# Kernel optimization log

Measured on AMD Instinct MI355X. Metric: run time of the kernel, lower is better.

Reference implementation:

```python
import jax, jax.numpy as jnp
import numpy as np

B, N, DIM, H, DH = 2, 1024, 2048, 16, 128
MAX_POS = 16
QK_SCALE = 10.0  # qk_norm_scale (replaces dim_head**-0.5 when qk_norm=True)
NEG = -1e30  # large negative mask value (sigmoid -> 0, softmax -> 0)

def rotate_half(x):
    # interleaved pair rotation: '... (d r) -> ... d r', r=2
    shape = x.shape
    xr = x.reshape(shape[:-1] + (shape[-1] // 2, 2))
    x1, x2 = xr[..., 0], xr[..., 1]
    return jnp.stack((-x2, x1), axis=-1).reshape(shape)

def setup_inputs() -> dict:
    key = jax.random.key(0)
    ks = jax.random.split(key, 10)
    # proper rotary frequencies, repeat-interleaved to match rotate_half's pair layout
    half = DH // 2
    inv_freq = 1.0 / (10000.0 ** (np.arange(half, dtype=np.float32) / half))
    freqs = np.repeat(np.outer(np.arange(N, dtype=np.float32), inv_freq), 2, axis=-1)  # [N, DH]
    sd = 0.02
    return {
        'x': jax.random.normal(ks[0], (B, N, DIM), jnp.float32),
        'rotary_freqs': jnp.asarray(freqs),
        'w_q': jax.random.normal(ks[1], (DIM, H * DH), jnp.float32) * sd,
        'w_k': jax.random.normal(ks[2], (DIM, H * DH), jnp.float32) * sd,
        'w_v': jax.random.normal(ks[3], (DIM, H * DH), jnp.float32) * sd,
        'cope_emb': jax.random.normal(ks[4], (MAX_POS, DH), jnp.float32) * sd,  # CoPE pos_emb (nonzero for testing)
        'th_pre': jnp.eye(H, dtype=jnp.float32) + jax.random.normal(ks[5], (H, H), jnp.float32) * sd,
        'th_post': jnp.eye(H, dtype=jnp.float32) + jax.random.normal(ks[6], (H, H), jnp.float32) * sd,
        'w_vgate': jax.random.normal(ks[7], (DIM, H * DH), jnp.float32) * sd,
        'b_vgate': jnp.full((H * DH,), 10.0, jnp.float32),
        'w_hgate': jax.random.normal(ks[8], (DIM, H), jnp.float32) * sd,
        'b_hgate': jnp.full((H,), 10.0, jnp.float32),
        'w_out': jax.random.normal(ks[9], (H * DH, DIM), jnp.float32) * sd,
    }

def reference(x, rotary_freqs, w_q, w_k, w_v, cope_emb, th_pre, th_post, w_vgate, b_vgate, w_hgate, b_hgate, w_out):
    b, n, _ = x.shape
    to_heads = lambda t: t.reshape(b, n, H, DH).transpose(0, 2, 1, 3)  # b h n d
    q = to_heads(x @ w_q)
    k = to_heads(x @ w_k)
    v = to_heads(x @ w_v)
    # qk l2-norm (groups=1), then fixed qk_norm_scale
    q = q / jnp.maximum(jnp.linalg.norm(q, axis=-1, keepdims=True), 1e-12)
    k = k / jnp.maximum(jnp.linalg.norm(k, axis=-1, keepdims=True), 1e-12)
    # rotary embedding (scale=1, rot_dim == dim_head)
    cos, sin = jnp.cos(rotary_freqs), jnp.sin(rotary_freqs)
    q = q * cos + rotate_half(q) * sin
    k = k * cos + rotate_half(k) * sin
    sim = jnp.einsum('bhid,bhjd->bhij', q, k) * QK_SCALE
    sim = jnp.einsum('hg,bgij->bhij', th_pre, sim)  # pre-softmax talking heads (1x1 conv over heads)
    causal = jnp.triu(jnp.ones((n, n), dtype=bool), 1)
    sim = jnp.where(causal, NEG, sim)
    # ---- CoPE (linear interpolation path) ----
    gates = jax.nn.sigmoid(sim)  # masked entries -> 0
    pos = jnp.flip(jnp.cumsum(jnp.flip(gates, -1), axis=-1), -1)  # reverse cumsum over j
    pos = jnp.minimum(pos, MAX_POS - 1.0)
    logits_int = jnp.einsum('bhnd,pd->bhnp', q, cope_emb)
    pos_floor = jnp.floor(pos)
    w_interp = pos - pos_floor
    lc = jnp.take_along_axis(logits_int, jnp.ceil(pos).astype(jnp.int32), axis=-1)
    lf = jnp.take_along_axis(logits_int, pos_floor.astype(jnp.int32), axis=-1)
    sim = sim + lc * w_interp + lf * (1.0 - w_interp)
    # ------------------------------------------
    attn = jax.nn.softmax(sim, axis=-1)
    attn = jnp.einsum('hg,bgij->bhij', th_post, attn)  # post-softmax talking heads
    out = jnp.einsum('bhij,bhjd->bhid', attn, v)
    # per-head value gate
    head_gate = jax.nn.sigmoid(x @ w_hgate + b_hgate)  # b n h
    out = out * head_gate.transpose(0, 2, 1)[..., None]
    out = out.transpose(0, 2, 1, 3).reshape(b, n, H * DH)
    # elementwise value gate (sigmoid, bias init 10)
    out = out * jax.nn.sigmoid(x @ w_vgate + b_vgate)
    return out @ w_out
```

## Files before the change

kernel.cpp:

```cpp
#include <hip/hip_runtime.h>
#include <hip/hip_fp16.h>

typedef unsigned short u16;
typedef __attribute__((ext_vector_type(4))) float f32x4;
typedef __attribute__((ext_vector_type(8))) _Float16 f16x8;
typedef __attribute__((ext_vector_type(4))) _Float16 f16x4;
typedef __attribute__((ext_vector_type(8))) unsigned short u16x8;
typedef __attribute__((ext_vector_type(4))) unsigned short u16x4;

#define DEVI __device__ __forceinline__
#define MASKV (-1000.0f)

DEVI u16 f2h(float f){ __half h = __float2half(f); return __half_as_ushort(h); }
DEVI float h2f(u16 v){ return __half2float(__ushort_as_half(v)); }
DEVI float sigm(float s){ float e = __expf(-fabsf(s)); return (s >= 0.f) ? 1.f/(1.f+e) : e/(1.f+e); }

DEVI void async16(const void* g, void* l){
  __builtin_amdgcn_global_load_lds((__attribute__((address_space(1))) const unsigned int*)g,
                                   (__attribute__((address_space(3))) unsigned int*)l, 16, 0, 0);
}

struct Acc { f32x4 a[4][4]; };
DEVI void acc_zero(Acc& a){
  f32x4 z = {0.f,0.f,0.f,0.f};
  #pragma unroll
  for (int i=0;i<4;i++)
    #pragma unroll
    for (int j=0;j<4;j++) a.a[i][j] = z;
}

DEVI void gemm_core(const u16* __restrict__ A, int lda, const u16* __restrict__ Bt, int ldb,
                    int K, u16* As, u16* Bs, Acc& acc, int tid)
{
  int w = tid >> 6, l = tid & 63;
  int q = l >> 4, m = l & 15;
  int wm = w & 1, wn = w >> 1;
  for (int k0 = 0; k0 < K; k0 += 32){
    __syncthreads();
    #pragma unroll
    for (int p = 0; p < 2; p++){
      int row = w*32 + p*16 + (l>>2);
      async16(A  + (size_t)row*lda + k0 + (l&3)*8, As + (w*32 + p*16)*32);
      async16(Bt + (size_t)row*ldb + k0 + (l&3)*8, Bs + (w*32 + p*16)*32);
    }
    __syncthreads();
    f16x8 af[4], bf[4];
    #pragma unroll
    for (int t = 0; t < 4; t++){
      af[t] = *(const f16x8*)(As + (wm*64 + t*16 + m)*32 + q*8);
      bf[t] = *(const f16x8*)(Bs + (wn*64 + t*16 + m)*32 + q*8);
    }
    #pragma unroll
    for (int i = 0; i < 4; i++)
      #pragma unroll
      for (int j = 0; j < 4; j++)
        acc.a[i][j] = __builtin_amdgcn_mfma_f32_16x16x32_f16(af[i], bf[j], acc.a[i][j], 0, 0, 0);
  }
}

struct PrepArgs {
  const float* src[7];
  u16* dst[7];
  int C[7];
};
__global__ __launch_bounds__(256) void k_prep(PrepArgs p){
  __shared__ u16 t[32][33];
  int z = blockIdx.z;
  if (z == 0){
    int i = ((blockIdx.y*64 + blockIdx.x)*256 + threadIdx.x)*4;
    f32x4 v = *(const f32x4*)(p.src[0] + i);
    u16x4 o;
    #pragma unroll
    for (int z2=0; z2<4; z2++) o[z2] = f2h(v[z2]);
    *(u16x4*)(p.dst[0] + i) = o;
    return;
  }
  const float* src = p.src[z]; u16* dst = p.dst[z];
  int R = 2048, C = p.C[z];
  int c0 = blockIdx.x*32, r0 = blockIdx.y*32;
  if (c0 >= C) return;
  int tx = threadIdx.x & 31, ty = threadIdx.x >> 5;
  #pragma unroll
  for (int i = ty; i < 32; i += 8){
    int r = r0 + i, c = c0 + tx;
    if (r < R && c < C) t[i][tx] = f2h(src[(size_t)r*C + c]);
  }
  __syncthreads();
  #pragma unroll
  for (int i = ty; i < 32; i += 8){
    int rr = c0 + i, cc = r0 + tx;
    if (rr < C && cc < R) dst[(size_t)rr*R + cc] = t[tx][i];
  }
}

__global__ __launch_bounds__(256) void k_transpose_h(const u16* __restrict__ src, u16* __restrict__ dst,
    int R, int C, long sps, long dps){
  __shared__ u16 t[32][33];
  src += (size_t)blockIdx.z * sps; dst += (size_t)blockIdx.z * dps;
  int c0 = blockIdx.x*32, r0 = blockIdx.y*32;
  int tx = threadIdx.x & 31, ty = threadIdx.x >> 5;
  #pragma unroll
  for (int i = ty; i < 32; i += 8){
    int r = r0 + i, c = c0 + tx;
    if (r < R && c < C) t[i][tx] = src[(size_t)r*C + c];
  }
  __syncthreads();
  #pragma unroll
  for (int i = ty; i < 32; i += 8){
    int rr = c0 + i, cc = r0 + tx;
    if (rr < C && cc < R) dst[(size_t)rr*R + cc] = t[tx][i];
  }
}

struct ProjArgs {
  const u16* xh;
  const u16* wT0; const u16* wT1; const u16* wT2; const u16* wT3;
  u16* q; u16* k; u16* v; u16* vg;
  const float* bvg;
};
__global__ __launch_bounds__(256) void k_proj(ProjArgs p){
  __shared__ __align__(16) u16 As[4096];
  __shared__ __align__(16) u16 Bs[4096];
  int z = blockIdx.z;
  const u16* wT = (z==0) ? p.wT0 : (z==1) ? p.wT1 : (z==2) ? p.wT2 : p.wT3;
  int tid = threadIdx.x;
  Acc acc; acc_zero(acc);
  const u16* A  = p.xh + (size_t)blockIdx.x*128*2048;
  const u16* Bt = wT   + (size_t)blockIdx.y*128*2048;
  gemm_core(A, 2048, Bt, 2048, 2048, As, Bs, acc, tid);
  int w = tid>>6, l = tid&63, q4 = l>>4, m = l&15, wm = w&1, wn = w>>1;
  #pragma unroll
  for (int ti=0; ti<4; ti++)
  #pragma unroll
  for (int tj=0; tj<4; tj++)
  #pragma unroll
  for (int r=0; r<4; r++){
    int trow = blockIdx.x*128 + wm*64 + ti*16 + q4*4 + r;
    int col  = blockIdx.y*128 + wn*64 + tj*16 + m;
    float v = acc.a[ti][tj][r];
    if (z == 3){
      float sg = sigm(v + p.bvg[col]);
      p.vg[(size_t)trow*2048 + col] = f2h(sg);
    } else {
      int b = trow >> 10, i = trow & 1023, h = col >> 7, d = col & 127;
      u16* dst = (z==0) ? p.q : (z==1) ? p.k : p.v;
      dst[(((size_t)(b*16 + h))*1024 + i)*128 + d] = f2h(v);
    }
  }
}

__global__ __launch_bounds__(256) void k_hgate(const u16* __restrict__ xh, const u16* __restrict__ whgT,
    const float* __restrict__ bhg, float* __restrict__ hg){
  __shared__ float red[4][256];
  int tid = threadIdx.x, w = tid>>6, l = tid&63, q = l>>4, m = l&15;
  int t0 = blockIdx.x*16;
  f32x4 acc = {0.f,0.f,0.f,0.f};
  const u16* xr = xh   + (size_t)(t0 + m)*2048 + w*512;
  const u16* br = whgT + (size_t)m*2048 + w*512;
  #pragma unroll 4
  for (int k = 0; k < 512; k += 32){
    f16x8 a = *(const f16x8*)(xr + k + q*8);
    f16x8 b = *(const f16x8*)(br + k + q*8);
    acc = __builtin_amdgcn_mfma_f32_16x16x32_f16(a, b, acc, 0, 0, 0);
  }
  #pragma unroll
  for (int r = 0; r < 4; r++) red[w][(q*4+r)*16 + m] = acc[r];
  __syncthreads();
  float v = red[0][tid] + red[1][tid] + red[2][tid] + red[3][tid];
  int tl = tid >> 4, h = tid & 15;
  hg[(size_t)(t0 + tl)*16 + h] = sigm(v + bhg[h]);
}

__global__ __launch_bounds__(256) void k_normrope(u16* __restrict__ qb, u16* __restrict__ kb,
    const float* __restrict__ freqs, const float* __restrict__ cope, float* __restrict__ L){
  __shared__ float ce[2048];
  int tid = threadIdx.x;
  for (int i2 = tid; i2 < 2048; i2 += 256) ce[i2] = cope[i2];
  __syncthreads();
  int w = tid >> 6, l = tid & 63;
  int r = blockIdx.x*4 + w;
  int isq = (r < 32768) ? 1 : 0;
  int rr = isq ? r : r - 32768;
  int i = rr & 1023;
  u16* base = (isq ? qb : kb) + (size_t)rr*128;
  float v0 = h2f(base[2*l]), v1 = h2f(base[2*l+1]);
  float ss = v0*v0 + v1*v1;
  #pragma unroll
  for (int off = 1; off < 64; off <<= 1) ss += __shfl_xor(ss, off);
  float rn = 1.f / fmaxf(sqrtf(ss), 1e-12f);
  v0 *= rn; v1 *= rn;
  float f = freqs[i*128 + 2*l];
  float sn, cs; sincosf(f, &sn, &cs);
  float o0 = v0*cs - v1*sn, o1 = v1*cs + v0*sn;
  base[2*l] = f2h(o0); base[2*l+1] = f2h(o1);
  if (isq){
    #pragma unroll
    for (int p = 0; p < 16; p++){
      float part = o0*ce[p*128 + 2*l] + o1*ce[p*128 + 2*l + 1];
      #pragma unroll
      for (int off = 1; off < 64; off <<= 1) part += __shfl_xor(part, off);
      if (l == p) L[(size_t)rr*16 + p] = part;
    }
  }
}

__global__ __launch_bounds__(256) void k_qk(const u16* __restrict__ qb, const u16* __restrict__ kb,
    u16* __restrict__ S){
  __shared__ __align__(16) u16 As[4096];
  __shared__ __align__(16) u16 Bs[4096];
  int tile = blockIdx.x, bh = blockIdx.y;
  int it = 0;
  #pragma unroll
  for (int t2 = 1; t2 < 8; t2++) if (tile >= (t2*(t2+1))/2) it = t2;
  int jt = tile - (it*(it+1))/2;
  const u16* A  = qb + (size_t)bh*131072 + (size_t)it*16384;
  const u16* Bt = kb + (size_t)bh*131072 + (size_t)jt*16384;
  Acc acc; acc_zero(acc);
  gemm_core(A, 128, Bt, 128, 128, As, Bs, acc, threadIdx.x);
  int tid = threadIdx.x, w = tid>>6, l = tid&63, q = l>>4, m = l&15, wm = w&1, wn = w>>1;
  u16* dst = S + ((size_t)bh*36 + tile)*16384;
  #pragma unroll
  for (int ti=0; ti<4; ti++)
  #pragma unroll
  for (int tj=0; tj<4; tj++)
  #pragma unroll
  for (int r=0; r<4; r++){
    int iloc = wm*64 + ti*16 + q*4 + r;
    int jloc = wn*64 + tj*16 + m;
    float v = acc.a[ti][tj][r] * 10.f;
    if (jt*128 + jloc > it*128 + iloc) v = MASKV;
    dst[(size_t)iloc*128 + jloc] = f2h(v);
  }
}

struct CopeArgs { const u16* S; const float* L; const float* thpre; u16* Sout; float* ml; };
__global__ __launch_bounds__(1024) void k_cope(CopeArgs pa){
  __shared__ u16 raw[16*276];
  __shared__ float thsh[256];
  __shared__ float Lsh[1024];
  int b = blockIdx.y;
  int i0 = (int)(gridDim.x - 1 - blockIdx.x) * 4;
  int tid = threadIdx.x, w = tid>>6, l = tid&63;
  int h = w;
  if (tid < 256) thsh[tid] = pa.thpre[tid];
  Lsh[tid] = pa.L[ ((size_t)((b*16 + (tid>>6))*1024) + i0 + ((tid>>4)&3))*16 + (tid&15) ];
  __syncthreads();
  float th_r[16];
  #pragma unroll
  for (int g = 0; g < 16; g++) th_r[g] = thsh[h*16 + g];
  int ii = l >> 4, j0 = (l & 15)*4;
  int i = i0 + ii, it1 = i >> 7, iloc = i & 127;
  const float* Lrow = Lsh + h*64 + ii*16;
  float carry = 0.f, mrun = -1e30f, lrun = 0.f;
  int tmax = (i0 + 3) >> 6;
  for (int t = tmax; t >= 0; t--){
    int jt1 = (t*64) >> 7, jo = (t*64) & 127;
    __syncthreads();
    {
      int e = tid*4;
      int g = e >> 8, r = e & 255;
      int si = r >> 6, j = r & 63;
      int irow = i0 + si; int it2 = irow >> 7, il2 = irow & 127;
      const u16* src = pa.S + ((size_t)((b*16+g)*36 + (it2*(it2+1))/2 + jt1))*16384
                           + (size_t)il2*128 + jo + j;
      *(u16x4*)(raw + g*276 + si*68 + j) = *(const u16x4*)src;
    }
    __syncthreads();
    float s0=0.f, s1=0.f, s2=0.f, s3=0.f;
    #pragma unroll
    for (int g = 0; g < 16; g++){
      u16x4 v = *(const u16x4*)(raw + g*276 + ii*68 + j0);
      float tg = th_r[g];
      s0 += tg*h2f(v[0]); s1 += tg*h2f(v[1]); s2 += tg*h2f(v[2]); s3 += tg*h2f(v[3]);
    }
    float g0 = sigm(s0), g1 = sigm(s1), g2 = sigm(s2), g3 = sigm(s3);
    float c3 = g3, c2 = g2 + c3, c1 = g1 + c2, c0 = g0 + c1;
    float T = c0, Tacc = T;
    #pragma unroll
    for (int off = 1; off < 16; off <<= 1){
      float tv = __shfl(Tacc, (l + off) & 63);
      if (((l & 15) + off) < 16) Tacc += tv;
    }
    float Rh = Tacc - T;
    float rowtot = __shfl(Tacc, l & 48);
    float sf[4];
    float cc[4] = {c0, c1, c2, c3};
    float ssv[4] = {s0, s1, s2, s3};
    #pragma unroll
    for (int c = 0; c < 4; c++){
      float pos = fminf(cc[c] + Rh + carry, 15.f);
      float pf = floorf(pos);
      float wi = pos - pf;
      int ic = (int)ceilf(pos), ifl = (int)pf;
      float v = ssv[c] + Lrow[ic]*wi + Lrow[ifl]*(1.f - wi);
      sf[c] = v;
    }
    carry += rowtot;
    u16x4 ov;
    #pragma unroll
    for (int c = 0; c < 4; c++){ ov[c] = f2h(sf[c]); sf[c] = h2f(ov[c]); }
    *(u16x4*)(pa.Sout + ((size_t)((b*16+h)*36 + (it1*(it1+1))/2 + jt1))*16384
              + (size_t)iloc*128 + jo + j0) = ov;
    float M = fmaxf(fmaxf(sf[0], sf[1]), fmaxf(sf[2], sf[3]));
    #pragma unroll
    for (int off = 1; off < 16; off <<= 1) M = fmaxf(M, __shfl_xor(M, off));
    float mnew = fmaxf(mrun, M);
    float es = __expf(fminf(sf[0]-mnew,0.f)) + __expf(fminf(sf[1]-mnew,0.f))
             + __expf(fminf(sf[2]-mnew,0.f)) + __expf(fminf(sf[3]-mnew,0.f));
    #pragma unroll
    for (int off = 1; off < 16; off <<= 1) es += __shfl_xor(es, off);
    lrun = lrun*__expf(fminf(mrun - mnew, 0.f)) + es;
    mrun = mnew;
  }
  if ((l & 15) == 0){
    size_t bix = (size_t)(b*16 + h)*1024 + i0 + ii;
    pa.ml[bix] = mrun;
    pa.ml[32768 + bix] = 1.f/fmaxf(lrun, 1e-30f);
  }
}

struct PostArgs { const u16* S; const float* ml; const float* thpost; u16* Sout; };
__global__ __launch_bounds__(256) void k_postmix(PostArgs pa){
  __shared__ u16 at[16*1040];
  __shared__ _Float16 thsh[256];
  __shared__ float mh[128], rlh[128];
  int tile = blockIdx.x >> 4, sub = blockIdx.x & 15, b = blockIdx.y;
  int it = 0;
  #pragma unroll
  for (int t2=1; t2<8; t2++) if (tile >= (t2*(t2+1))/2) it = t2;
  int tid = threadIdx.x;
  thsh[tid] = (_Float16)pa.thpost[tid];
  if (tid < 128){
    int g = tid >> 3, ii = tid & 7;
    size_t ix = (size_t)(b*16+g)*1024 + it*128 + sub*8 + ii;
    mh[tid] = pa.ml[ix]; rlh[tid] = pa.ml[32768 + ix];
  }
  __syncthreads();
  {
    int g = tid >> 4, l16 = tid & 15;
    const u16* src = pa.S + ((size_t)((b*16+g)*36 + tile))*16384 + sub*1024;
    #pragma unroll
    for (int c = 0; c < 16; c++){
      int e = c*64 + l16*4;
      int ii = e >> 7;
      float mm = mh[g*8+ii], rr = rlh[g*8+ii];
      u16x4 sv = *(const u16x4*)(src + e);
      u16x4 o;
      #pragma unroll
      for (int z2=0; z2<4; z2++) o[z2] = f2h(__expf(fminf(h2f(sv[z2]) - mm, 0.f)) * rr);
      *(u16x4*)(at + g*1040 + e) = o;
    }
  }
  __syncthreads();
  int h = tid >> 4, c16 = tid & 15;
  _Float16 th_h[16];
  #pragma unroll
  for (int g = 0; g < 16; g++) th_h[g] = thsh[h*16 + g];
  u16* dst = pa.Sout + ((size_t)((b*16+h)*36 + tile))*16384 + sub*1024;
  #pragma unroll
  for (int k = 0; k < 16; k++){
    int e = c16*4 + k*64;
    f16x4 a = {0,0,0,0};
    #pragma unroll
    for (int g = 0; g < 16; g++){
      f16x4 v = *(const f16x4*)(at + g*1040 + e);
      a += v * th_h[g];
    }
    *(f16x4*)(dst + e) = a;
  }
}

struct PvArgs { const u16* S; const u16* vT; const float* hg; const u16* vg; u16* gated; };
__global__ __launch_bounds__(256) void k_pv(PvArgs pa){
  __shared__ __align__(16) u16 As[2048];
  __shared__ __align__(16) u16 Bs[4096];
  int bh = blockIdx.y, b = bh >> 4, h = bh & 15;
  int isub = (int)(gridDim.x - 1 - blockIdx.x);
  int i0 = isub * 64;
  int it1 = i0 >> 7, ibase = i0 & 127;
  int nk = (i0 + 64) / 32;
  const u16* abase = pa.S  + ((size_t)(bh*36 + (it1*(it1+1))/2))*16384;
  const u16* vt    = pa.vT + (size_t)bh*131072;
  int tid = threadIdx.x, w = tid>>6, l = tid&63, q = l>>4, m = l&15, wm = w&1, wn = w>>1;
  f32x4 acc[2][4];
  { f32x4 z = {0.f,0.f,0.f,0.f};
    #pragma unroll
    for (int i2=0;i2<2;i2++)
      #pragma unroll
      for (int j2=0;j2<4;j2++) acc[i2][j2] = z; }
  for (int ks = 0; ks < nk; ks++){
    __syncthreads();
    {
      int row = w*16 + (l>>2);
      async16(abase + (size_t)(ks>>2)*16384 + (size_t)(ibase + row)*128 + (ks&3)*32 + (l&3)*8,
              As + (w*16)*32);
    }
    #pragma unroll
    for (int p2=0; p2<2; p2++){
      int row = w*32 + p2*16 + (l>>2);
      async16(vt + (size_t)row*1024 + ks*32 + (l&3)*8, Bs + (w*32 + p2*16)*32);
    }
    __syncthreads();
    f16x8 af[2], bf[4];
    #pragma unroll
    for (int t=0;t<2;t++) af[t] = *(const f16x8*)(As + (wm*32 + t*16 + m)*32 + q*8);
    #pragma unroll
    for (int t=0;t<4;t++) bf[t] = *(const f16x8*)(Bs + (wn*64 + t*16 + m)*32 + q*8);
    #pragma unroll
    for (int i2=0;i2<2;i2++)
      #pragma unroll
      for (int j2=0;j2<4;j2++)
        acc[i2][j2] = __builtin_amdgcn_mfma_f32_16x16x32_f16(af[i2], bf[j2], acc[i2][j2], 0, 0, 0);
  }
  #pragma unroll
  for (int ti=0; ti<2; ti++)
  #pragma unroll
  for (int tj=0; tj<4; tj++)
  #pragma unroll
  for (int r=0; r<4; r++){
    int i = i0 + wm*32 + ti*16 + q*4 + r;
    int d = wn*64 + tj*16 + m;
    int tok = b*1024 + i;
    float v = acc[ti][tj][r] * pa.hg[(size_t)tok*16 + h] * h2f(pa.vg[(size_t)tok*2048 + h*128 + d]);
    if (v != v) v = 333.f;
    pa.gated[(size_t)tok*2048 + h*128 + d] = f2h(v);
  }
}

__global__ __launch_bounds__(256) void k_out(const u16* __restrict__ gated, const u16* __restrict__ woT,
    float* __restrict__ out){
  __shared__ __align__(16) u16 As[4096];
  __shared__ __align__(16) u16 Bs[4096];
  Acc acc; acc_zero(acc);
  gemm_core(gated + (size_t)blockIdx.x*128*2048, 2048,
            woT   + (size_t)blockIdx.y*128*2048, 2048, 2048, As, Bs, acc, threadIdx.x);
  int tid = threadIdx.x, w = tid>>6, l = tid&63, q = l>>4, m = l&15, wm = w&1, wn = w>>1;
  #pragma unroll
  for (int ti=0; ti<4; ti++)
  #pragma unroll
  for (int tj=0; tj<4; tj++)
  #pragma unroll
  for (int r=0; r<4; r++){
    int trow = blockIdx.x*128 + wm*64 + ti*16 + q*4 + r;
    int col  = blockIdx.y*128 + wn*64 + tj*16 + m;
    float o = acc.a[ti][tj][r];
    if (o != o) o = 911.f;
    out[(size_t)trow*2048 + col] = o;
  }
}

extern "C" void kernel_launch(void* const* d_in, const int* in_sizes, int n_in,
                              void* d_out, int out_size, void* d_ws, size_t ws_size,
                              hipStream_t stream){
  const float* x      = (const float*)d_in[0];
  const float* freqs  = (const float*)d_in[1];
  const float* w_q    = (const float*)d_in[2];
  const float* w_k    = (const float*)d_in[3];
  const float* w_v    = (const float*)d_in[4];
  const float* cope   = (const float*)d_in[5];
  const float* thpre  = (const float*)d_in[6];
  const float* thpost = (const float*)d_in[7];
  const float* w_vg   = (const float*)d_in[8];
  const float* b_vg   = (const float*)d_in[9];
  const float* w_hg   = (const float*)d_in[10];
  const float* b_hg   = (const float*)d_in[11];
  const float* w_out  = (const float*)d_in[12];

  char* ws = (char*)d_ws;
  size_t off = 0;
  auto alloc = [&](size_t bytes)->char*{ char* r = ws + off; off += (bytes + 255) & ~(size_t)255; return r; };
  u16*   xh    = (u16*)  alloc(8388608);
  u16*   wqT   = (u16*)  alloc(8388608);
  u16*   wkT   = (u16*)  alloc(8388608);
  u16*   wvT   = (u16*)  alloc(8388608);
  u16*   wvgT  = (u16*)  alloc(8388608);
  u16*   woT   = (u16*)  alloc(8388608);
  u16*   whgT  = (u16*)  alloc(65536);
  u16*   qb    = (u16*)  alloc(8388608);
  u16*   kb    = (u16*)  alloc(8388608);
  u16*   vb    = (u16*)  alloc(8388608);
  u16*   vTT   = (u16*)  alloc(8388608);
  u16*   vg    = (u16*)  alloc(8388608);
  u16*   gated = (u16*)  alloc(8388608);
  float* L     = (float*)alloc(2097152);
  float* hg    = (float*)alloc(131072);
  float* ml    = (float*)alloc(262144);
  u16*   S     = (u16*)  alloc(37748736);

  dim3 b256(256);
  PrepArgs pp;
  pp.src[0]=x;    pp.dst[0]=xh;   pp.C[0]=2048;
  pp.src[1]=w_q;  pp.dst[1]=wqT;  pp.C[1]=2048;
  pp.src[2]=w_k;  pp.dst[2]=wkT;  pp.C[2]=2048;
  pp.src[3]=w_v;  pp.dst[3]=wvT;  pp.C[3]=2048;
  pp.src[4]=w_vg; pp.dst[4]=wvgT; pp.C[4]=2048;
  pp.src[5]=w_out;pp.dst[5]=woT;  pp.C[5]=2048;
  pp.src[6]=w_hg; pp.dst[6]=whgT; pp.C[6]=16;
  k_prep<<<dim3(64,64,7), b256, 0, stream>>>(pp);

  ProjArgs pa{ xh, wqT, wkT, wvT, wvgT, qb, kb, vb, vg, b_vg };
  k_proj<<<dim3(16,16,4), b256, 0, stream>>>(pa);
  k_hgate<<<dim3(128), b256, 0, stream>>>(xh, whgT, b_hg, hg);
  k_transpose_h<<<dim3(4,32,32), b256, 0, stream>>>(vb, vTT, 1024, 128, 131072L, 131072L);
  k_normrope<<<dim3(16384), b256, 0, stream>>>(qb, kb, freqs, cope, L);
  k_qk<<<dim3(36,32), b256, 0, stream>>>(qb, kb, S);
  CopeArgs ca{ S, L, thpre, S, ml };
  k_cope<<<dim3(256,2), dim3(1024), 0, stream>>>(ca);
  PostArgs po{ S, ml, thpost, S };
  k_postmix<<<dim3(576,2), b256, 0, stream>>>(po);
  PvArgs pv{ S, vTT, hg, vg, gated };
  k_pv<<<dim3(16,32), b256, 0, stream>>>(pv);
  k_out<<<dim3(16,16), b256, 0, stream>>>(gated, woT, (float*)d_out);
}
```

Before: 509.8 us.

## Retile QK, PV and output GEMMs to 64-row blocks with wider K staging

k_qk now gives each block one 64-row query strip, loads Q once into LDS and loops over all causal key tiles, replacing one block per 128x128 triangle tile. k_pv stages full 128-wide K chunks (four 32-slices) per barrier pair, cutting synchronisation count. k_out shrinks the tile to 64x128, doubling the grid to 512 blocks for better CU occupancy. The aim is fewer barriers and more parallelism, at the cost of larger LDS use, which may limit occupancy, and more redundant loads of the weights in k_out.

```diff
diff --git a/kernel.cpp b/kernel.cpp
--- a/kernel.cpp
+++ b/kernel.cpp
@@ -206,30 +206,64 @@
 
 __global__ __launch_bounds__(256) void k_qk(const u16* __restrict__ qb, const u16* __restrict__ kb,
     u16* __restrict__ S){
-  __shared__ __align__(16) u16 As[4096];
-  __shared__ __align__(16) u16 Bs[4096];
-  int tile = blockIdx.x, bh = blockIdx.y;
-  int it = 0;
-  #pragma unroll
-  for (int t2 = 1; t2 < 8; t2++) if (tile >= (t2*(t2+1))/2) it = t2;
-  int jt = tile - (it*(it+1))/2;
-  const u16* A  = qb + (size_t)bh*131072 + (size_t)it*16384;
-  const u16* Bt = kb + (size_t)bh*131072 + (size_t)jt*16384;
-  Acc acc; acc_zero(acc);
-  gemm_core(A, 128, Bt, 128, 128, As, Bs, acc, threadIdx.x);
+  __shared__ __align__(16) u16 As[8192];
+  __shared__ __align__(16) u16 Bs[16384];
+  int bh = blockIdx.y;
+  int bx = 15 - (int)blockIdx.x;
+  int i0 = bx*64, it = bx >> 1;
+  int njt = (bx + 2) >> 1;
   int tid = threadIdx.x, w = tid>>6, l = tid&63, q = l>>4, m = l&15, wm = w&1, wn = w>>1;
-  u16* dst = S + ((size_t)bh*36 + tile)*16384;
-  #pragma unroll
-  for (int ti=0; ti<4; ti++)
-  #pragma unroll
-  for (int tj=0; tj<4; tj++)
-  #pragma unroll
-  for (int r=0; r<4; r++){
-    int iloc = wm*64 + ti*16 + q*4 + r;
-    int jloc = wn*64 + tj*16 + m;
-    float v = acc.a[ti][tj][r] * 10.f;
-    if (jt*128 + jloc > it*128 + iloc) v = MASKV;
-    dst[(size_t)iloc*128 + jloc] = f2h(v);
+  const u16* qbase = qb + (size_t)bh*131072;
+  const u16* kbase = kb + (size_t)bh*131072;
+  #pragma unroll
+  for (int sub = 0; sub < 4; sub++){
+    int row = w*16 + (l>>2);
+    async16(qbase + (size_t)(i0 + row)*128 + sub*32 + (l&3)*8, As + sub*2048 + (w*16)*32);
+  }
+  u16* dstbase = S + ((size_t)bh*36 + (it*(it+1))/2)*16384 + (size_t)((bx&1)*64)*128;
+  for (int jt = 0; jt < njt; jt++){
+    __syncthreads();
+    #pragma unroll
+    for (int sub = 0; sub < 4; sub++)
+      #pragma unroll
+      for (int p = 0; p < 2; p++){
+        int row = w*32 + p*16 + (l>>2);
+        async16(kbase + (size_t)(jt*128 + row)*128 + sub*32 + (l&3)*8,
+                Bs + sub*4096 + (w*32 + p*16)*32);
+      }
+    __syncthreads();
+    f32x4 acc[2][4];
+    { f32x4 z = {0.f,0.f,0.f,0.f};
+      #pragma unroll
+      for (int a2=0;a2<2;a2++)
+        #pragma unroll
+        for (int b2=0;b2<4;b2++) acc[a2][b2] = z; }
+    #pragma unroll
+    for (int kc = 0; kc < 4; kc++){
+      f16x8 af[2], bf[4];
+      #pragma unroll
+      for (int t = 0; t < 2; t++) af[t] = *(const f16x8*)(As + kc*2048 + (wm*32 + t*16 + m)*32 + q*8);
+      #pragma unroll
+      for (int t = 0; t < 4; t++) bf[t] = *(const f16x8*)(Bs + kc*4096 + (wn*64 + t*16 + m)*32 + q*8);
+      #pragma unroll
+      for (int a2 = 0; a2 < 2; a2++)
+        #pragma unroll
+        for (int b2 = 0; b2 < 4; b2++)
+          acc[a2][b2] = __builtin_amdgcn_mfma_f32_16x16x32_f16(af[a2], bf[b2], acc[a2][b2], 0, 0, 0);
+    }
+    u16* dst = dstbase + (size_t)jt*16384;
+    #pragma unroll
+    for (int ti=0; ti<2; ti++)
+    #pragma unroll
+    for (int tj=0; tj<4; tj++)
+    #pragma unroll
+    for (int r=0; r<4; r++){
+      int iloc = wm*32 + ti*16 + q*4 + r;
+      int jloc = wn*64 + tj*16 + m;
+      float v = acc[ti][tj][r] * 10.f;
+      if (jt*128 + jloc > i0 + iloc) v = MASKV;
+      dst[(size_t)iloc*128 + jloc] = f2h(v);
+    }
   }
 }
 
@@ -372,45 +406,49 @@
 
 struct PvArgs { const u16* S; const u16* vT; const float* hg; const u16* vg; u16* gated; };
 __global__ __launch_bounds__(256) void k_pv(PvArgs pa){
-  __shared__ __align__(16) u16 As[2048];
-  __shared__ __align__(16) u16 Bs[4096];
+  __shared__ __align__(16) u16 As[8192];
+  __shared__ __align__(16) u16 Bs[16384];
   int bh = blockIdx.y, b = bh >> 4, h = bh & 15;
-  int isub = (int)(gridDim.x - 1 - blockIdx.x);
-  int i0 = isub * 64;
-  int it1 = i0 >> 7, ibase = i0 & 127;
-  int nk = (i0 + 64) / 32;
-  const u16* abase = pa.S  + ((size_t)(bh*36 + (it1*(it1+1))/2))*16384;
+  int bx = 15 - (int)blockIdx.x;
+  int i0 = bx*64, it = bx >> 1;
+  int nc = (bx + 2) >> 1;
+  int tid = threadIdx.x, w = tid>>6, l = tid&63, q = l>>4, m = l&15, wm = w&1, wn = w>>1;
+  const u16* abase = pa.S + ((size_t)bh*36 + (it*(it+1))/2)*16384 + (size_t)((bx&1)*64)*128;
   const u16* vt    = pa.vT + (size_t)bh*131072;
-  int tid = threadIdx.x, w = tid>>6, l = tid&63, q = l>>4, m = l&15, wm = w&1, wn = w>>1;
   f32x4 acc[2][4];
   { f32x4 z = {0.f,0.f,0.f,0.f};
     #pragma unroll
-    for (int i2=0;i2<2;i2++)
-      #pragma unroll
-      for (int j2=0;j2<4;j2++) acc[i2][j2] = z; }
-  for (int ks = 0; ks < nk; ks++){
-    __syncthreads();
-    {
+    for (int a2=0;a2<2;a2++)
+      #pragma unroll
+      for (int b2=0;b2<4;b2++) acc[a2][b2] = z; }
+  for (int jc = 0; jc < nc; jc++){
+    __syncthreads();
+    #pragma unroll
+    for (int sub = 0; sub < 4; sub++){
       int row = w*16 + (l>>2);
-      async16(abase + (size_t)(ks>>2)*16384 + (size_t)(ibase + row)*128 + (ks&3)*32 + (l&3)*8,
-              As + (w*16)*32);
-    }
-    #pragma unroll
-    for (int p2=0; p2<2; p2++){
-      int row = w*32 + p2*16 + (l>>2);
-      async16(vt + (size_t)row*1024 + ks*32 + (l&3)*8, Bs + (w*32 + p2*16)*32);
-    }
-    __syncthreads();
-    f16x8 af[2], bf[4];
-    #pragma unroll
-    for (int t=0;t<2;t++) af[t] = *(const f16x8*)(As + (wm*32 + t*16 + m)*32 + q*8);
-    #pragma unroll
-    for (int t=0;t<4;t++) bf[t] = *(const f16x8*)(Bs + (wn*64 + t*16 + m)*32 + q*8);
-    #pragma unroll
-    for (int i2=0;i2<2;i2++)
-      #pragma unroll
-      for (int j2=0;j2<4;j2++)
-        acc[i2][j2] = __builtin_amdgcn_mfma_f32_16x16x32_f16(af[i2], bf[j2], acc[i2][j2], 0, 0, 0);
+      async16(abase + (size_t)jc*16384 + (size_t)row*128 + sub*32 + (l&3)*8,
+              As + sub*2048 + (w*16)*32);
+      #pragma unroll
+      for (int p = 0; p < 2; p++){
+        int brow = w*32 + p*16 + (l>>2);
+        async16(vt + (size_t)brow*1024 + jc*128 + sub*32 + (l&3)*8,
+                Bs + sub*4096 + (w*32 + p*16)*32);
+      }
+    }
+    __syncthreads();
+    #pragma unroll
+    for (int kc = 0; kc < 4; kc++){
+      f16x8 af[2], bf[4];
+      #pragma unroll
+      for (int t = 0; t < 2; t++) af[t] = *(const f16x8*)(As + kc*2048 + (wm*32 + t*16 + m)*32 + q*8);
+      #pragma unroll
+      for (int t = 0; t < 4; t++) bf[t] = *(const f16x8*)(Bs + kc*4096 + (wn*64 + t*16 + m)*32 + q*8);
+      #pragma unroll
+      for (int a2 = 0; a2 < 2; a2++)
+        #pragma unroll
+        for (int b2 = 0; b2 < 4; b2++)
+          acc[a2][b2] = __builtin_amdgcn_mfma_f32_16x16x32_f16(af[a2], bf[b2], acc[a2][b2], 0, 0, 0);
+    }
   }
   #pragma unroll
   for (int ti=0; ti<2; ti++)
@@ -429,21 +467,50 @@
 
 __global__ __launch_bounds__(256) void k_out(const u16* __restrict__ gated, const u16* __restrict__ woT,
     float* __restrict__ out){
-  __shared__ __align__(16) u16 As[4096];
+  __shared__ __align__(16) u16 As[2048];
   __shared__ __align__(16) u16 Bs[4096];
-  Acc acc; acc_zero(acc);
-  gemm_core(gated + (size_t)blockIdx.x*128*2048, 2048,
-            woT   + (size_t)blockIdx.y*128*2048, 2048, 2048, As, Bs, acc, threadIdx.x);
+  int bx = blockIdx.x;
+  int by = blockIdx.y;
+  int trow0 = by*64, c0 = bx*128;
   int tid = threadIdx.x, w = tid>>6, l = tid&63, q = l>>4, m = l&15, wm = w&1, wn = w>>1;
-  #pragma unroll
-  for (int ti=0; ti<4; ti++)
+  f32x4 acc[2][4];
+  { f32x4 z = {0.f,0.f,0.f,0.f};
+    #pragma unroll
+    for (int a2=0;a2<2;a2++)
+      #pragma unroll
+      for (int b2=0;b2<4;b2++) acc[a2][b2] = z; }
+  for (int k0 = 0; k0 < 2048; k0 += 32){
+    __syncthreads();
+    {
+      int row = w*16 + (l>>2);
+      async16(gated + (size_t)(trow0 + row)*2048 + k0 + (l&3)*8, As + (w*16)*32);
+    }
+    #pragma unroll
+    for (int p = 0; p < 2; p++){
+      int row = w*32 + p*16 + (l>>2);
+      async16(woT + (size_t)(c0 + row)*2048 + k0 + (l&3)*8, Bs + (w*32 + p*16)*32);
+    }
+    __syncthreads();
+    f16x8 af[2], bf[4];
+    #pragma unroll
+    for (int t = 0; t < 2; t++) af[t] = *(const f16x8*)(As + (wm*32 + t*16 + m)*32 + q*8);
+    #pragma unroll
+    for (int t = 0; t < 4; t++) bf[t] = *(const f16x8*)(Bs + (wn*64 + t*16 + m)*32 + q*8);
+    #pragma unroll
+    for (int a2 = 0; a2 < 2; a2++)
+      #pragma unroll
+      for (int b2 = 0; b2 < 4; b2++)
+        acc[a2][b2] = __builtin_amdgcn_mfma_f32_16x16x32_f16(af[a2], bf[b2], acc[a2][b2], 0, 0, 0);
+  }
+  #pragma unroll
+  for (int ti=0; ti<2; ti++)
   #pragma unroll
   for (int tj=0; tj<4; tj++)
   #pragma unroll
   for (int r=0; r<4; r++){
-    int trow = blockIdx.x*128 + wm*64 + ti*16 + q*4 + r;
-    int col  = blockIdx.y*128 + wn*64 + tj*16 + m;
-    float o = acc.a[ti][tj][r];
+    int trow = trow0 + wm*32 + ti*16 + q*4 + r;
+    int col  = c0 + wn*64 + tj*16 + m;
+    float o = acc[ti][tj][r];
     if (o != o) o = 911.f;
     out[(size_t)trow*2048 + col] = o;
   }
@@ -503,12 +570,12 @@
   k_hgate<<<dim3(128), b256, 0, stream>>>(xh, whgT, b_hg, hg);
   k_transpose_h<<<dim3(4,32,32), b256, 0, stream>>>(vb, vTT, 1024, 128, 131072L, 131072L);
   k_normrope<<<dim3(16384), b256, 0, stream>>>(qb, kb, freqs, cope, L);
-  k_qk<<<dim3(36,32), b256, 0, stream>>>(qb, kb, S);
+  k_qk<<<dim3(16,32), b256, 0, stream>>>(qb, kb, S);
   CopeArgs ca{ S, L, thpre, S, ml };
   k_cope<<<dim3(256,2), dim3(1024), 0, stream>>>(ca);
   PostArgs po{ S, ml, thpost, S };
   k_postmix<<<dim3(576,2), b256, 0, stream>>>(po);
   PvArgs pv{ S, vTT, hg, vg, gated };
   k_pv<<<dim3(16,32), b256, 0, stream>>>(pv);
-  k_out<<<dim3(16,16), b256, 0, stream>>>(gated, woT, (float*)d_out);
-}
+  k_out<<<dim3(16,32), b256, 0, stream>>>(gated, woT, (float*)d_out);
+}
```

After: 498.9 us. 2.1% less time.
